# Kernel tuning notes

Measured on AMD Instinct MI355X. Metric: run time of the kernel, lower is better.

## Reference

```python
import jax, jax.numpy as jnp
import numpy as np

P_TOP = 0.1          # fraction of brightest pixels for atmosphere
LEC_K = 3            # local-extremum conv kernel size (w=3 in forward)
HID = 64             # hidden channels of stand-in Net


def _conv2d(x, w, pad):
    return jax.lax.conv_general_dilated(
        x, w, window_strides=(1, 1), padding=[(pad, pad), (pad, pad)],
        dimension_numbers=("NCHW", "OIHW", "NCHW"))


def _lec_weights(k, dtype):
    # LocalExtremumConv.init_weights: all +/-1/k^2 with +/-1 at the center
    base = jnp.full((1, 1, k, k), 1.0 / (k * k), dtype=dtype)
    base = base.at[0, 0, k // 2, k // 2].set(1.0)
    return -base, base  # (min_weights, max_weights)


def setup_inputs() -> dict:
    key = jax.random.key(0)
    ks = jax.random.split(key, 8)
    B, C, H, W = 8, 3, 512, 512
    x = jax.random.uniform(ks[0], (B, C, H, W), dtype=jnp.float32)
    s1 = 1.0 / np.sqrt(C * 9)
    s2 = 1.0 / np.sqrt(HID * 9)
    return {
        "x": x,
        "net_w1": jax.random.normal(ks[1], (HID, C, 3, 3), jnp.float32) * s1,
        "net_b1": jnp.zeros((HID,), jnp.float32),
        "net_w2": jax.random.normal(ks[2], (C, HID, 3, 3), jnp.float32) * s2,
        "net_b2": jnp.zeros((C,), jnp.float32),
        "color_w": jax.random.normal(ks[3], (3, 3), jnp.float32) * (1.0 / np.sqrt(3)),
        "color_b": jnp.zeros((3,), jnp.float32),
        "conv_w": jax.random.normal(ks[4], (4, 3, 1, 1), jnp.float32) * (1.0 / np.sqrt(3)),
        "conv_b": jnp.zeros((4,), jnp.float32),
    }


def reference(x, net_w1, net_b1, net_w2, net_b2, color_w, color_b, conv_w, conv_b):
    B, C, H, W = x.shape
    # --- stand-in Net: 3->64->3 conv enhancement, sigmoid output ---
    h = jax.nn.relu(_conv2d(x, net_w1, 1) + net_b1[None, :, None, None])
    img_high = jax.nn.sigmoid(_conv2d(h, net_w2, 1) + net_b2[None, :, None, None])
    # --- stand-in Color_pred: GAP -> linear -> sigmoid -> (B,3,1,1) gain ---
    color = jax.nn.sigmoid(x.mean(axis=(2, 3)) @ color_w.T + color_b)
    img_high = img_high * color[:, :, None, None]
    # --- 1x1 conv -> split K (1ch), Bias (3ch); residual correction ---
    feat = _conv2d(img_high, conv_w, 0) + conv_b[None, :, None, None]
    K, Bt = feat[:, 0:1], feat[:, 1:4]
    x_out = K * x - Bt + x
    # --- illumination channel: reflect pad + channel min/max + LEC convs ---
    pad = LEC_K // 2
    xp = jnp.pad(x_out, ((0, 0), (0, 0), (pad, pad), (pad, pad)), mode="reflect")
    x_max = xp.max(axis=1, keepdims=True)
    _, max_w = _lec_weights(LEC_K, x.dtype)
    bright = jax.nn.relu(_conv2d(x_max, max_w, 0))  # (B,1,H,W)
    # --- atmosphere: top-p% brightest pixels, gather + mean ---
    # NOTE: faithful to torch images.view(B,-1,C) on NCHW (layout-scrambled)
    flat_img = x_out.reshape(B, H * W, C)
    flat_bright = bright.reshape(B, H * W)
    num_pixels = int(P_TOP * H * W)
    _, idx = jax.lax.top_k(flat_bright, num_pixels)          # (B, num_pixels)
    picked = jnp.take_along_axis(flat_img, idx[:, :, None], axis=1)
    A = picked.mean(axis=1)                                   # (B, C)
    return (x_out, A)
```

## Files before the change

### kernel.cpp

```cpp
#include <hip/hip_runtime.h>
#include <hip/hip_bf16.h>

#define Hn 512
#define Wn 512
#define HWn (512 * 512)
#define KTOP 26214

typedef __attribute__((ext_vector_type(8))) short frag_ab;
typedef __attribute__((ext_vector_type(4))) float frag_cd;

__device__ __forceinline__ float sigf(float z) { return 1.0f / (1.0f + __expf(-z)); }

__device__ __forceinline__ short f2bf(float f) {
  unsigned u = __float_as_uint(f);
  u += 0x7FFFu + ((u >> 16) & 1u);
  return (short)(u >> 16);
}

__device__ __forceinline__ unsigned aload(const unsigned* p) {
  return __hip_atomic_load(p, __ATOMIC_RELAXED, __HIP_MEMORY_SCOPE_AGENT);
}

__global__ __launch_bounds__(256) void k_means(
    const float* __restrict__ x, float* __restrict__ means, unsigned* __restrict__ doneCnt,
    const float* __restrict__ w1, const float* __restrict__ b1, const float* __restrict__ w2,
    const float* __restrict__ cw, const float* __restrict__ cb,
    short* __restrict__ w1A, short* __restrict__ w2A, float* __restrict__ colorG)
{
  const int tid = threadIdx.x;
  __shared__ int lastS;
  int bc = blockIdx.x >> 5;
  int slice = blockIdx.x & 31;
  const float4* p = (const float4*)(x + bc * HWn + slice * 8192);
  float s = 0.f;
  for (int i = tid; i < 2048; i += 256) { float4 v = p[i]; s += v.x + v.y + v.z + v.w; }
  for (int off = 32; off > 0; off >>= 1) s += __shfl_down(s, off);
  if ((tid & 63) == 0) atomicAdd(&means[bc], s);
  __syncthreads();
  if (tid == 0) {
    unsigned tk = __hip_atomic_fetch_add(doneCnt, 1u, __ATOMIC_RELAXED, __HIP_MEMORY_SCOPE_AGENT);
    lastS = (tk == 767);
  }
  __syncthreads();
  if (!lastS) return;

  {
    int chunk = tid >> 6, lane = tid & 63;
    int m = lane & 15, q = lane >> 4;
    for (int j = 0; j < 8; ++j) {
      int k = q * 8 + j;
      float v = 0.f;
      if (k < 27) v = w1[(chunk * 16 + m) * 27 + k];
      else if (k == 27) v = b1[chunk * 16 + m];
      w1A[tid * 8 + j] = f2bf(v);
    }
  }
  for (int i = tid; i < 384; i += 256) {
    int step = i >> 6, lane = i & 63;
    int m = lane & 15, q = lane >> 4;
    int dx = step >> 1, half = step & 1;
    int dy = m / 3, oc = m - dy * 3;
    for (int j = 0; j < 8; ++j) {
      int ch = half * 32 + q * 8 + j;
      float v = (m < 9) ? w2[oc * 576 + ch * 9 + dy * 3 + dx] : 0.f;
      w2A[i * 8 + j] = f2bf(v);
    }
  }
  if (tid < 24) {
    int b = tid / 3, oc = tid % 3;
    float z = cb[oc];
    for (int j = 0; j < 3; ++j)
      z += (atomicAdd(&means[b * 3 + j], 0.f) * (1.0f / (float)HWn)) * cw[oc * 3 + j];
    colorG[tid] = sigf(z);
  }
}

__global__ __launch_bounds__(256, 4) void k_fused(
    const float* __restrict__ x,
    const float* __restrict__ b2, const float* __restrict__ convw, const float* __restrict__ convb,
    const short* __restrict__ w1Ag, const short* __restrict__ w2Ag,
    const float* __restrict__ colorG, float* __restrict__ out)
{
  __shared__ __align__(16) unsigned short xs[720];
  __shared__ __align__(16) unsigned short hb[180 * 72];
  __shared__ __align__(16) float dstore[10 * 162];
  __shared__ float b2s[3], colorS[3], cwS[12], cbS[4];

  const int tid = threadIdx.x;
  const int wid = tid >> 6, lane = tid & 63;
  const int n = lane & 15, q = lane >> 4;
  const int tx0 = blockIdx.x * 16, ty0 = blockIdx.y * 8;
  const int b = blockIdx.z;

  for (int i = tid; i < 720; i += 256) {
    int c = i / 240, r = i - c * 240;
    int yy = r / 20, xx = r - yy * 20;
    int gy = ty0 - 2 + yy, gx = tx0 - 2 + xx;
    float v = 0.f;
    if ((unsigned)gy < 512u && (unsigned)gx < 512u)
      v = x[(b * 3 + c) * HWn + (gy << 9) + gx];
    xs[i] = (unsigned short)f2bf(v);
  }
  if (tid < 3)  b2s[tid] = b2[tid];
  if (tid < 3)  colorS[tid] = colorG[b * 3 + tid];
  if (tid < 12) cwS[tid] = convw[tid];
  if (tid < 4)  cbS[tid] = convb[tid];

  frag_ab w1f[4];
#pragma unroll
  for (int ck = 0; ck < 4; ++ck) w1f[ck] = *(const frag_ab*)(w1Ag + (ck * 64 + lane) * 8);

  int kb[8], kf[8];
#pragma unroll
  for (int j = 0; j < 8; ++j) {
    int k = q * 8 + j;
    if (k < 27) { int ic = k / 9; int r = k - ic * 9; kb[j] = (ic * 240 + (r / 3) * 20 + (r % 3)) * 2; kf[j] = 0; }
    else if (k == 27) { kb[j] = 0; kf[j] = 1; }
    else { kb[j] = 0; kf[j] = 2; }
  }
  __syncthreads();

  for (int g = wid; g < 12; g += 4) {
    int pt = g * 16 + n;
    bool ptok = pt < 180;
    int ptc = ptok ? pt : 0;
    int pty = (ptc * 3641) >> 16;
    int ptx = ptc - pty * 18;
    int baseB = (pty * 20 + ptx) * 2;
    int gy = ty0 - 1 + pty, gx = tx0 - 1 + ptx;
    bool valid = ptok && (unsigned)gy < 512u && (unsigned)gx < 512u;
    frag_ab B;
#pragma unroll
    for (int j = 0; j < 8; ++j) {
      short v;
      if (kf[j] == 0) v = *(const short*)((const char*)xs + baseB + kb[j]);
      else v = (kf[j] == 1) ? (short)0x3F80 : (short)0;
      B[j] = v;
    }
#pragma unroll
    for (int ck = 0; ck < 4; ++ck) {
      frag_cd D = {0.f, 0.f, 0.f, 0.f};
      D = __builtin_amdgcn_mfma_f32_16x16x32_bf16(w1f[ck], B, D, 0, 0, 0);
      if (ptok) {
        float2 p01 = make_float2(fmaxf(D[0], 0.f), fmaxf(D[1], 0.f));
        float2 p23 = make_float2(fmaxf(D[2], 0.f), fmaxf(D[3], 0.f));
        __hip_bfloat162 c01 = __float22bfloat162_rn(p01);
        __hip_bfloat162 c23 = __float22bfloat162_rn(p23);
        unsigned lo = valid ? *(unsigned*)&c01 : 0u;
        unsigned hi = valid ? *(unsigned*)&c23 : 0u;
        uint2 v2; v2.x = lo; v2.y = hi;
        *(uint2*)(hb + pt * 72 + ck * 16 + q * 4) = v2;
      }
    }
  }

  frag_ab w2f[6];
#pragma unroll
  for (int i = 0; i < 6; ++i) w2f[i] = *(const frag_ab*)(w2Ag + (i * 64 + lane) * 8);
  __syncthreads();

  for (int r = wid; r < 10; r += 4) {
    frag_cd acc = {0.f, 0.f, 0.f, 0.f};
#pragma unroll
    for (int i = 0; i < 6; ++i) {
      int dx = i >> 1;
      int chb = (i & 1) * 64 + q * 16;
      frag_ab Bf = *(const frag_ab*)((const char*)hb + (r * 18 + n + dx) * 144 + chb);
      acc = __builtin_amdgcn_mfma_f32_16x16x32_bf16(w2f[i], Bf, acc, 0, 0, 0);
    }
    float* dp = dstore + r * 162 + n * 10 + q * 4;
    if (q < 2) {
      *(float2*)dp = make_float2(acc[0], acc[1]);
      *(float2*)(dp + 2) = make_float2(acc[2], acc[3]);
    } else if (q == 2) {
      dp[0] = acc[0];
    }
  }
  __syncthreads();

  if (tid < 128) {
    int y = tid >> 4, xcol = tid & 15;
    float a0 = b2s[0], a1 = b2s[1], a2 = b2s[2];
#pragma unroll
    for (int dy = 0; dy < 3; ++dy) {
      const float* dp = dstore + (y + dy) * 162 + xcol * 10 + dy * 3;
      a0 += dp[0]; a1 += dp[1]; a2 += dp[2];
    }
    float ih0 = colorS[0] * sigf(a0);
    float ih1 = colorS[1] * sigf(a1);
    float ih2 = colorS[2] * sigf(a2);
    float Kv = cwS[0] * ih0 + cwS[1]  * ih1 + cwS[2]  * ih2 + cbS[0];
    float f1 = cwS[3] * ih0 + cwS[4]  * ih1 + cwS[5]  * ih2 + cbS[1];
    float f2 = cwS[6] * ih0 + cwS[7]  * ih1 + cwS[8]  * ih2 + cbS[2];
    float f3 = cwS[9] * ih0 + cwS[10] * ih1 + cwS[11] * ih2 + cbS[3];
    float xc0 = __bfloat162float(*(const __hip_bfloat16*)&xs[0 * 240 + (y + 2) * 20 + (xcol + 2)]);
    float xc1 = __bfloat162float(*(const __hip_bfloat16*)&xs[1 * 240 + (y + 2) * 20 + (xcol + 2)]);
    float xc2 = __bfloat162float(*(const __hip_bfloat16*)&xs[2 * 240 + (y + 2) * 20 + (xcol + 2)]);
    int oi = ((ty0 + y) << 9) + (tx0 + xcol);
    out[(b * 3 + 0) * HWn + oi] = Kv * xc0 - f1 + xc0;
    out[(b * 3 + 1) * HWn + oi] = Kv * xc1 - f2 + xc1;
    out[(b * 3 + 2) * HWn + oi] = Kv * xc2 - f3 + xc2;
  }
}

__device__ __forceinline__ void softBarrier(unsigned* ctr) {
  __syncthreads();
  if (threadIdx.x == 0) {
    __hip_atomic_fetch_add(ctr, 1u, __ATOMIC_RELAXED, __HIP_MEMORY_SCOPE_AGENT);
    while (__hip_atomic_load(ctr, __ATOMIC_RELAXED, __HIP_MEMORY_SCOPE_AGENT) < 64u)
      __builtin_amdgcn_s_sleep(2);
  }
  __syncthreads();
}

__device__ void sel256(const unsigned* __restrict__ h, unsigned kneed,
                       unsigned* sm, unsigned* oBin, unsigned* oAbove)
{
  const int t = threadIdx.x;
  sm[t] = aload(&h[t]);
  __syncthreads();
  for (int d = 1; d < 256; d <<= 1) {
    unsigned add = (t + d < 256) ? sm[t + d] : 0u;
    __syncthreads();
    sm[t] += add;
    __syncthreads();
  }
  unsigned mine = sm[t];
  unsigned nxt = (t < 255) ? sm[t + 1] : 0u;
  if (mine >= kneed && nxt < kneed) { *oBin = (unsigned)t; *oAbove = nxt; }
  __syncthreads();
}

__device__ void sel4096(const unsigned* __restrict__ h, unsigned kneed,
                        unsigned* sm, unsigned* oBin, unsigned* oAbove)
{
  const int t = threadIdx.x;
  unsigned loc[16]; unsigned sum = 0;
#pragma unroll
  for (int i = 0; i < 16; ++i) { loc[i] = aload(&h[t * 16 + i]); sum += loc[i]; }
  sm[t] = sum;
  __syncthreads();
  for (int d = 1; d < 256; d <<= 1) {
    unsigned add = (t + d < 256) ? sm[t + d] : 0u;
    __syncthreads();
    sm[t] += add;
    __syncthreads();
  }
  unsigned mine = sm[t];
  unsigned nxt = (t < 255) ? sm[t + 1] : 0u;
  if (mine >= kneed && nxt < kneed) {
    unsigned acc = nxt;
    for (int i = 15; i >= 0; --i) {
      unsigned c = loc[i];
      if (acc + c >= kneed) { *oBin = (unsigned)(t * 16 + i); *oAbove = acc; break; }
      acc += c;
    }
  }
  __syncthreads();
}

__global__ __launch_bounds__(256) void k_tail(
    const float* __restrict__ outv, float* __restrict__ bright,
    unsigned* __restrict__ h1, unsigned* __restrict__ h12, unsigned* __restrict__ h3,
    unsigned* __restrict__ eqTaken, float* __restrict__ Asum,
    unsigned* __restrict__ barCtr, unsigned* __restrict__ doneCnt, float* __restrict__ outA)
{
  __shared__ __align__(16) float xm[10][516];
  __shared__ unsigned hh[4096];
  __shared__ unsigned sm[256];
  __shared__ unsigned sB1, sA1, sB2, sA2, sB3, sA3;
  __shared__ float red[4][3];
  __shared__ int lastA;

  const int tid = threadIdx.x;
  const int b = blockIdx.x >> 6, strip = blockIdx.x & 63;
  const int y0 = strip * 8;
  const float* op = outv + b * 3 * HWn;
  unsigned* bar = barCtr + b * 48;

  hh[tid] = 0;
  for (int idx = tid; idx < 1280; idx += 256) {
    int r = idx >> 7, seg = idx & 127;
    int gy = y0 - 1 + r; gy = (gy < 0) ? -gy : (gy > 511 ? 1022 - gy : gy);
    int c0 = seg * 4;
    const float* rp = op + (gy << 9) + c0;
    float4 v0 = *(const float4*)rp;
    float4 v1 = *(const float4*)(rp + HWn);
    float4 v2 = *(const float4*)(rp + 2 * HWn);
    xm[r][c0 + 1] = fmaxf(v0.x, fmaxf(v1.x, v2.x));
    xm[r][c0 + 2] = fmaxf(v0.y, fmaxf(v1.y, v2.y));
    xm[r][c0 + 3] = fmaxf(v0.z, fmaxf(v1.z, v2.z));
    xm[r][c0 + 4] = fmaxf(v0.w, fmaxf(v1.w, v2.w));
  }
  if (tid < 20) {
    int r = tid >> 1, side = tid & 1;
    int gy = y0 - 1 + r; gy = (gy < 0) ? -gy : (gy > 511 ? 1022 - gy : gy);
    int gx = side ? 510 : 1;
    float m = fmaxf(op[(gy << 9) + gx], fmaxf(op[HWn + (gy << 9) + gx], op[2 * HWn + (gy << 9) + gx]));
    xm[r][side ? 513 : 0] = m;
  }
  __syncthreads();
  {
    const int row = tid >> 5, cl = tid & 31;
#pragma unroll 4
    for (int i = 0; i < 16; ++i) {
      int c = cl + (i << 5);
      float s0 = xm[row][c]     + xm[row][c + 1]     + xm[row][c + 2];
      float s1 = xm[row + 1][c] + xm[row + 1][c + 1] + xm[row + 1][c + 2];
      float s2 = xm[row + 2][c] + xm[row + 2][c + 1] + xm[row + 2][c + 2];
      float s = (s0 + s1 + s2) * (1.f / 9.f) + xm[row + 1][c + 1] * (8.f / 9.f);
      s = fmaxf(s, 0.f);
      bright[b * HWn + ((y0 + row) << 9) + c] = s;
      atomicAdd(&hh[__float_as_uint(s) >> 24], 1u);
    }
  }
  __syncthreads();
  if (hh[tid]) atomicAdd(&h1[(b << 8) + tid], hh[tid]);
  softBarrier(bar);

  sel256(h1 + (b << 8), KTOP, sm, &sB1, &sA1);
  for (int i = tid; i < 4096; i += 256) hh[i] = 0;
  __syncthreads();
  const float4* bp = (const float4*)(bright + b * HWn + (y0 << 9));
  const unsigned sb1 = sB1;
#pragma unroll
  for (int it = 0; it < 4; ++it) {
    float4 v = bp[it * 256 + tid];
    unsigned u0 = __float_as_uint(v.x), u1 = __float_as_uint(v.y);
    unsigned u2 = __float_as_uint(v.z), u3 = __float_as_uint(v.w);
    if ((u0 >> 24) == sb1) atomicAdd(&hh[(u0 >> 12) & 0xFFFu], 1u);
    if ((u1 >> 24) == sb1) atomicAdd(&hh[(u1 >> 12) & 0xFFFu], 1u);
    if ((u2 >> 24) == sb1) atomicAdd(&hh[(u2 >> 12) & 0xFFFu], 1u);
    if ((u3 >> 24) == sb1) atomicAdd(&hh[(u3 >> 12) & 0xFFFu], 1u);
  }
  __syncthreads();
  for (int i = tid; i < 4096; i += 256)
    if (hh[i]) atomicAdd(&h12[(b << 12) + i], hh[i]);
  softBarrier(bar + 16);

  sel4096(h12 + (b << 12), KTOP - sA1, sm, &sB2, &sA2);
  const unsigned P20 = (sB1 << 12) | sB2;
#pragma unroll
  for (int it = 0; it < 4; ++it) {
    float4 v = bp[it * 256 + tid];
    unsigned u0 = __float_as_uint(v.x), u1 = __float_as_uint(v.y);
    unsigned u2 = __float_as_uint(v.z), u3 = __float_as_uint(v.w);
    if ((u0 >> 12) == P20) atomicAdd(&h3[(b << 12) + (u0 & 0xFFFu)], 1u);
    if ((u1 >> 12) == P20) atomicAdd(&h3[(b << 12) + (u1 & 0xFFFu)], 1u);
    if ((u2 >> 12) == P20) atomicAdd(&h3[(b << 12) + (u2 & 0xFFFu)], 1u);
    if ((u3 >> 12) == P20) atomicAdd(&h3[(b << 12) + (u3 & 0xFFFu)], 1u);
  }
  softBarrier(bar + 32);

  const unsigned kp3 = KTOP - sA1 - sA2;
  sel4096(h3 + (b << 12), kp3, sm, &sB3, &sA3);
  const unsigned T = (P20 << 12) | sB3;
  const unsigned ne = kp3 - sA3;
  float v0 = 0.f, v1 = 0.f, v2 = 0.f;
  for (int it = 0; it < 16; ++it) {
    int pix = (y0 << 9) + it * 256 + tid;
    unsigned bits = __float_as_uint(bright[b * HWn + pix]);
    bool take = bits > T;
    if (bits == T) {
      if (aload(&eqTaken[b * 16]) < ne) {
        unsigned old = atomicAdd(&eqTaken[b * 16], 1u);
        take = old < ne;
      }
    }
    if (take) {
      v0 += op[3 * pix];
      v1 += op[3 * pix + 1];
      v2 += op[3 * pix + 2];
    }
  }
  for (int off = 32; off > 0; off >>= 1) {
    v0 += __shfl_down(v0, off);
    v1 += __shfl_down(v1, off);
    v2 += __shfl_down(v2, off);
  }
  int w = tid >> 6;
  if ((tid & 63) == 0) { red[w][0] = v0; red[w][1] = v1; red[w][2] = v2; }
  __syncthreads();
  if (tid == 0) {
    atomicAdd(&Asum[b * 3 + 0], red[0][0] + red[1][0] + red[2][0] + red[3][0]);
    atomicAdd(&Asum[b * 3 + 1], red[0][1] + red[1][1] + red[2][1] + red[3][1]);
    atomicAdd(&Asum[b * 3 + 2], red[0][2] + red[1][2] + red[2][2] + red[3][2]);
  }
  __syncthreads();
  if (tid == 0) {
    unsigned tk = __hip_atomic_fetch_add(doneCnt, 1u, __ATOMIC_RELAXED, __HIP_MEMORY_SCOPE_AGENT);
    lastA = (tk == 511);
  }
  __syncthreads();
  if (lastA && tid < 24)
    outA[3 * HWn * 8 + tid] = atomicAdd(&Asum[tid], 0.f) * (1.0f / (float)KTOP);
}

extern "C" void kernel_launch(void* const* d_in, const int* in_sizes, int n_in,
                              void* d_out, int out_size, void* d_ws, size_t ws_size,
                              hipStream_t stream)
{
  const float* x     = (const float*)d_in[0];
  const float* w1    = (const float*)d_in[1];
  const float* b1    = (const float*)d_in[2];
  const float* w2    = (const float*)d_in[3];
  const float* b2    = (const float*)d_in[4];
  const float* cw    = (const float*)d_in[5];
  const float* cb    = (const float*)d_in[6];
  const float* convw = (const float*)d_in[7];
  const float* convb = (const float*)d_in[8];
  float* out = (float*)d_out;
  char* ws = (char*)d_ws;

  float*    bright    = (float*)(ws);
  unsigned* h1        = (unsigned*)(ws + 8388608);
  unsigned* h12       = (unsigned*)(ws + 8396800);
  unsigned* h3        = (unsigned*)(ws + 8527872);
  float*    Asum      = (float*)(ws + 8658944);
  unsigned* eqTaken   = (unsigned*)(ws + 8659040);
  float*    means     = (float*)(ws + 8659552);
  unsigned* meansDone = (unsigned*)(ws + 8659648);
  unsigned* accumDone = (unsigned*)(ws + 8659680);
  unsigned* barCtr    = (unsigned*)(ws + 8659712);
  short*    w1Ag      = (short*)(ws + 8661248);
  short*    w2Ag      = (short*)(ws + 8665344);
  float*    colorG    = (float*)(ws + 8683776);

  hipMemsetAsync(ws + 8388608, 0, 8661248 - 8388608, stream);

  k_means<<<768, 256, 0, stream>>>(x, means, meansDone, w1, b1, w2, cw, cb, w1Ag, w2Ag, colorG);
  k_fused<<<dim3(32, 64, 8), 256, 0, stream>>>(x, b2, convw, convb, w1Ag, w2Ag, colorG, out);
  k_tail<<<512, 256, 0, stream>>>(out, bright, h1, h12, h3, eqTaken, Asum, barCtr, accumDone, out);
}
```

Measured before the change: 275.5 us.

## Keep brightness in LDS, seed MFMA with bias, alias dstore onto hidden buffer

k_tail now keeps each block's 4096 brightness values in shared memory instead of writing them to global and reading them back twice, which removes that global round trip. In k_fused, the conv1 bias is loaded into the MFMA accumulator instead of being carried as a constant-one K-slot. The input halo is loaded as four floats per thread, and the second-conv partial-sum store reuses the hidden-activation LDS buffer so more blocks can be resident (launch bound raised to 5). The extra 16KB of LDS per block in k_tail may reduce its occupancy. Reusing the hb buffer for the partials depends on the __syncthreads placement being correct.

```diff
diff --git a/kernel.cpp b/kernel.cpp
--- a/kernel.cpp
+++ b/kernel.cpp
@@ -49,9 +49,7 @@
     int m = lane & 15, q = lane >> 4;
     for (int j = 0; j < 8; ++j) {
       int k = q * 8 + j;
-      float v = 0.f;
-      if (k < 27) v = w1[(chunk * 16 + m) * 27 + k];
-      else if (k == 27) v = b1[chunk * 16 + m];
+      float v = (k < 27) ? w1[(chunk * 16 + m) * 27 + k] : 0.f;
       w1A[tid * 8 + j] = f2bf(v);
     }
   }
@@ -75,15 +73,15 @@
   }
 }
 
-__global__ __launch_bounds__(256, 4) void k_fused(
-    const float* __restrict__ x,
+__global__ __launch_bounds__(256, 5) void k_fused(
+    const float* __restrict__ x, const float* __restrict__ b1,
     const float* __restrict__ b2, const float* __restrict__ convw, const float* __restrict__ convb,
     const short* __restrict__ w1Ag, const short* __restrict__ w2Ag,
     const float* __restrict__ colorG, float* __restrict__ out)
 {
   __shared__ __align__(16) unsigned short xs[720];
-  __shared__ __align__(16) unsigned short hb[180 * 72];
-  __shared__ __align__(16) float dstore[10 * 162];
+  __shared__ __align__(16) unsigned short hb[12960];
+  __shared__ float bs[64];
   __shared__ float b2s[3], colorS[3], cwS[12], cbS[4];
 
   const int tid = threadIdx.x;
@@ -92,15 +90,22 @@
   const int tx0 = blockIdx.x * 16, ty0 = blockIdx.y * 8;
   const int b = blockIdx.z;
 
-  for (int i = tid; i < 720; i += 256) {
-    int c = i / 240, r = i - c * 240;
-    int yy = r / 20, xx = r - yy * 20;
-    int gy = ty0 - 2 + yy, gx = tx0 - 2 + xx;
-    float v = 0.f;
-    if ((unsigned)gy < 512u && (unsigned)gx < 512u)
-      v = x[(b * 3 + c) * HWn + (gy << 9) + gx];
-    xs[i] = (unsigned short)f2bf(v);
-  }
+  if (tid < 180) {
+    int c = tid / 60, rem = tid - c * 60;
+    int yy = rem / 5, xq = (rem - yy * 5) * 4;
+    int gy = ty0 - 2 + yy, gx0 = tx0 - 2 + xq;
+    bool rowok = (unsigned)gy < 512u;
+    const float* rp = x + (b * 3 + c) * HWn + (gy << 9) + gx0;
+    float v0 = (rowok && (unsigned)(gx0 + 0) < 512u) ? rp[0] : 0.f;
+    float v1 = (rowok && (unsigned)(gx0 + 1) < 512u) ? rp[1] : 0.f;
+    float v2 = (rowok && (unsigned)(gx0 + 2) < 512u) ? rp[2] : 0.f;
+    float v3 = (rowok && (unsigned)(gx0 + 3) < 512u) ? rp[3] : 0.f;
+    __hip_bfloat162 c01 = __float22bfloat162_rn(make_float2(v0, v1));
+    __hip_bfloat162 c23 = __float22bfloat162_rn(make_float2(v2, v3));
+    uint2 v2w; v2w.x = *(unsigned*)&c01; v2w.y = *(unsigned*)&c23;
+    *(uint2*)(xs + c * 240 + yy * 20 + xq) = v2w;
+  }
+  if (tid < 64) bs[tid] = b1[tid];
   if (tid < 3)  b2s[tid] = b2[tid];
   if (tid < 3)  colorS[tid] = colorG[b * 3 + tid];
   if (tid < 12) cwS[tid] = convw[tid];
@@ -110,15 +115,21 @@
 #pragma unroll
   for (int ck = 0; ck < 4; ++ck) w1f[ck] = *(const frag_ab*)(w1Ag + (ck * 64 + lane) * 8);
 
-  int kb[8], kf[8];
+  int kb[8];
 #pragma unroll
   for (int j = 0; j < 8; ++j) {
     int k = q * 8 + j;
-    if (k < 27) { int ic = k / 9; int r = k - ic * 9; kb[j] = (ic * 240 + (r / 3) * 20 + (r % 3)) * 2; kf[j] = 0; }
-    else if (k == 27) { kb[j] = 0; kf[j] = 1; }
-    else { kb[j] = 0; kf[j] = 2; }
-  }
-  __syncthreads();
+    int kk = (k < 27) ? k : (k - 27);
+    int ic = kk / 9; int r = kk - ic * 9;
+    kb[j] = (ic * 240 + (r / 3) * 20 + (r % 3)) * 2;
+  }
+  __syncthreads();
+
+  float biasr[4][4];
+#pragma unroll
+  for (int ck = 0; ck < 4; ++ck)
+#pragma unroll
+    for (int r = 0; r < 4; ++r) biasr[ck][r] = bs[ck * 16 + q * 4 + r];
 
   for (int g = wid; g < 12; g += 4) {
     int pt = g * 16 + n;
@@ -131,15 +142,11 @@
     bool valid = ptok && (unsigned)gy < 512u && (unsigned)gx < 512u;
     frag_ab B;
 #pragma unroll
-    for (int j = 0; j < 8; ++j) {
-      short v;
-      if (kf[j] == 0) v = *(const short*)((const char*)xs + baseB + kb[j]);
-      else v = (kf[j] == 1) ? (short)0x3F80 : (short)0;
-      B[j] = v;
-    }
+    for (int j = 0; j < 8; ++j)
+      B[j] = *(const short*)((const char*)xs + baseB + kb[j]);
 #pragma unroll
     for (int ck = 0; ck < 4; ++ck) {
-      frag_cd D = {0.f, 0.f, 0.f, 0.f};
+      frag_cd D = {biasr[ck][0], biasr[ck][1], biasr[ck][2], biasr[ck][3]};
       D = __builtin_amdgcn_mfma_f32_16x16x32_bf16(w1f[ck], B, D, 0, 0, 0);
       if (ptok) {
         float2 p01 = make_float2(fmaxf(D[0], 0.f), fmaxf(D[1], 0.f));
@@ -168,7 +175,7 @@
       frag_ab Bf = *(const frag_ab*)((const char*)hb + (r * 18 + n + dx) * 144 + chb);
       acc = __builtin_amdgcn_mfma_f32_16x16x32_bf16(w2f[i], Bf, acc, 0, 0, 0);
     }
-    float* dp = dstore + r * 162 + n * 10 + q * 4;
+    float* dp = (float*)(hb + r * 1296) + n * 10 + q * 4;
     if (q < 2) {
       *(float2*)dp = make_float2(acc[0], acc[1]);
       *(float2*)(dp + 2) = make_float2(acc[2], acc[3]);
@@ -183,7 +190,7 @@
     float a0 = b2s[0], a1 = b2s[1], a2 = b2s[2];
 #pragma unroll
     for (int dy = 0; dy < 3; ++dy) {
-      const float* dp = dstore + (y + dy) * 162 + xcol * 10 + dy * 3;
+      const float* dp = (const float*)(hb + (y + dy) * 1296) + xcol * 10 + dy * 3;
       a0 += dp[0]; a1 += dp[1]; a2 += dp[2];
     }
     float ih0 = colorS[0] * sigf(a0);
@@ -260,12 +267,13 @@
 }
 
 __global__ __launch_bounds__(256) void k_tail(
-    const float* __restrict__ outv, float* __restrict__ bright,
+    const float* __restrict__ outv,
     unsigned* __restrict__ h1, unsigned* __restrict__ h12, unsigned* __restrict__ h3,
     unsigned* __restrict__ eqTaken, float* __restrict__ Asum,
     unsigned* __restrict__ barCtr, unsigned* __restrict__ doneCnt, float* __restrict__ outA)
 {
   __shared__ __align__(16) float xm[10][516];
+  __shared__ __align__(16) float brightS[4096];
   __shared__ unsigned hh[4096];
   __shared__ unsigned sm[256];
   __shared__ unsigned sB1, sA1, sB2, sA2, sB3, sA3;
@@ -310,7 +318,7 @@
       float s2 = xm[row + 2][c] + xm[row + 2][c + 1] + xm[row + 2][c + 2];
       float s = (s0 + s1 + s2) * (1.f / 9.f) + xm[row + 1][c + 1] * (8.f / 9.f);
       s = fmaxf(s, 0.f);
-      bright[b * HWn + ((y0 + row) << 9) + c] = s;
+      brightS[(row << 9) + c] = s;
       atomicAdd(&hh[__float_as_uint(s) >> 24], 1u);
     }
   }
@@ -321,7 +329,7 @@
   sel256(h1 + (b << 8), KTOP, sm, &sB1, &sA1);
   for (int i = tid; i < 4096; i += 256) hh[i] = 0;
   __syncthreads();
-  const float4* bp = (const float4*)(bright + b * HWn + (y0 << 9));
+  const float4* bp = (const float4*)brightS;
   const unsigned sb1 = sB1;
 #pragma unroll
   for (int it = 0; it < 4; ++it) {
@@ -358,8 +366,9 @@
   const unsigned ne = kp3 - sA3;
   float v0 = 0.f, v1 = 0.f, v2 = 0.f;
   for (int it = 0; it < 16; ++it) {
-    int pix = (y0 << 9) + it * 256 + tid;
-    unsigned bits = __float_as_uint(bright[b * HWn + pix]);
+    int li = it * 256 + tid;
+    int pix = (y0 << 9) + li;
+    unsigned bits = __float_as_uint(brightS[li]);
     bool take = bits > T;
     if (bits == T) {
       if (aload(&eqTaken[b * 16]) < ne) {
@@ -412,7 +421,6 @@
   float* out = (float*)d_out;
   char* ws = (char*)d_ws;
 
-  float*    bright    = (float*)(ws);
   unsigned* h1        = (unsigned*)(ws + 8388608);
   unsigned* h12       = (unsigned*)(ws + 8396800);
   unsigned* h3        = (unsigned*)(ws + 8527872);
@@ -429,6 +437,6 @@
   hipMemsetAsync(ws + 8388608, 0, 8661248 - 8388608, stream);
 
   k_means<<<768, 256, 0, stream>>>(x, means, meansDone, w1, b1, w2, cw, cb, w1Ag, w2Ag, colorG);
-  k_fused<<<dim3(32, 64, 8), 256, 0, stream>>>(x, b2, convw, convb, w1Ag, w2Ag, colorG, out);
-  k_tail<<<512, 256, 0, stream>>>(out, bright, h1, h12, h3, eqTaken, Asum, barCtr, accumDone, out);
-}
+  k_fused<<<dim3(32, 64, 8), 256, 0, stream>>>(x, b1, b2, convw, convb, w1Ag, w2Ag, colorG, out);
+  k_tail<<<512, 256, 0, stream>>>(out, h1, h12, h3, eqTaken, Asum, barCtr, accumDone, out);
+}
```

Result: faster. 260.5 us (-5.5%).
